# Optimization experiments

Hardware: AMD Instinct MI355X
Metric: run time of the kernel (lower is better)

Reference implementation:

```python
import jax, jax.numpy as jnp
import numpy as np

SEGMENT_LENGTHS = (512, 1024, 2048)
DILATION_RATES = (1, 2, 4)


def _dilated_attention(q, k, v):
    """LongNet-style dilated segment attention.

    Faithful to RingDilatedAttentionHybridFixed._fallback_forward (ring_size=1,
    non-causal, eval mode): for each (segment_length, dilation_rate) pair the
    sequence is tiled into segments; queries attend to K/V gathered at strided
    (dilated) positions start + i*dilation within the sequence; indices past
    seq_len are masked out (the torch code drops them). Each group writes the
    full output buffer, so later groups overwrite earlier ones, exactly as in
    the source loop.
    """
    B, N, H, D = q.shape
    scale = D ** -0.5
    out = jnp.zeros_like(q)
    for seg_len, dil in zip(SEGMENT_LENGTHS, DILATION_RATES):
        seg = min(seg_len, N)
        nseg = N // seg  # N chosen divisible by every segment length
        qg = q.reshape(B, nseg, seg, H, D)
        # dilated kv indices per segment: start + i*dilation  -> [nseg, seg]
        idx = (jnp.arange(nseg) * seg)[:, None] + jnp.arange(seg)[None, :] * dil
        valid = idx < N
        idxc = jnp.minimum(idx, N - 1)
        kg = k[:, idxc]  # [B, nseg, seg, H, D]
        vg = v[:, idxc]
        scores = jnp.einsum('bnqhd,bnkhd->bnhqk', qg, kg) * scale
        scores = jnp.where(valid[None, :, None, None, :], scores, -jnp.inf)
        attn = jax.nn.softmax(scores, axis=-1)
        seg_out = jnp.einsum('bnhqk,bnkhd->bnqhd', attn, vg)
        # each group covers all positions -> whole-output overwrite (as in torch)
        out = seg_out.reshape(B, N, H, D)
    return out


def setup_inputs() -> dict:
    key = jax.random.key(0)
    kq, kk, kv = jax.random.split(key, 3)
    B, N, H, D = 1, 4096, 16, 64
    q = jax.random.normal(kq, (B, N, H, D), dtype=jnp.float32)
    k = jax.random.normal(kk, (B, N, H, D), dtype=jnp.float32)
    v = jax.random.normal(kv, (B, N, H, D), dtype=jnp.float32)
    return {"q": q, "k": k, "v": v}


def reference(q, k, v):
    return _dilated_attention(q, k, v)
```

## Files before the change

### kernel.cpp

```cpp
#include <hip/hip_runtime.h>
#include <hip/hip_bf16.h>
#include <stdint.h>


#define NH   16
#define HD   64
#define KMAX 1024

typedef __attribute__((ext_vector_type(8)))  short s16x8;
typedef __attribute__((ext_vector_type(4)))  float f32x4;
typedef __attribute__((ext_vector_type(16))) float f32x16;

__device__ __forceinline__ uint cvtpk(float lo, float hi) {
    uint r;
    asm("v_cvt_pk_bf16_f32 %0, %1, %2" : "=v"(r) : "v"(lo), "v"(hi));
    return r;
}

__device__ __forceinline__ void swap32(uint& a, uint& b) {
    asm volatile("v_permlane32_swap_b32 %0, %1" : "+v"(a), "+v"(b));
}

__device__ __forceinline__ float fexp2(float x) {
#if __has_builtin(__builtin_amdgcn_exp2f)
    return __builtin_amdgcn_exp2f(x);
#else
    return exp2f(x);
#endif
}

__device__ __forceinline__ void async_load16(const ushort* g, ushort* l) {
    __builtin_amdgcn_global_load_lds(
        (const __attribute__((address_space(1))) void*)g,
        (__attribute__((address_space(3))) void*)l, 16, 0, 0);
}

__device__ __forceinline__ int swz8(int row) { return (row ^ (row >> 3)) & 7; }

__global__ __launch_bounds__(256) void prep_kernel(
    const float* __restrict__ kin, const float* __restrict__ vin,
    ushort* __restrict__ Kb, ushort* __restrict__ Vt)
{
    int bid = blockIdx.x;
    int h   = bid >> 4;
    int ib  = bid & 15;
    int i0  = ib * 64;

    int t  = threadIdx.x;
    int il = t >> 2;
    int d0 = (t & 3) * 16;
    int i  = i0 + il;
    int pos = i * 4;

    const float* ks = kin + (size_t)pos * (NH*HD) + h * HD + d0;
    const float* vs = vin + (size_t)pos * (NH*HD) + h * HD + d0;

    union { uint u[8]; ushort s[16]; uint4 q4[2]; } kb, vb;
    #pragma unroll
    for (int j = 0; j < 4; ++j) {
        float4 a = ((const float4*)ks)[j];
        float4 b = ((const float4*)vs)[j];
        kb.u[2*j]   = cvtpk(a.x, a.y);
        kb.u[2*j+1] = cvtpk(a.z, a.w);
        vb.u[2*j]   = cvtpk(b.x, b.y);
        vb.u[2*j+1] = cvtpk(b.z, b.w);
    }
    size_t kdst = ((size_t)h * KMAX + i) * HD + d0;
    ((uint4*)(Kb + kdst))[0] = kb.q4[0];
    ((uint4*)(Kb + kdst))[1] = kb.q4[1];

    __shared__ ushort vl[64 * 72];
    #pragma unroll
    for (int j = 0; j < 16; ++j) vl[il * 72 + d0 + j] = vb.s[j];
    __syncthreads();

    int d  = t >> 2;
    int ic = (t & 3) * 16;
    __attribute__((aligned(16))) ushort ob[16];
    #pragma unroll
    for (int j = 0; j < 16; ++j) ob[j] = vl[(ic + j) * 72 + d];
    size_t vdst = ((size_t)h * HD + d) * KMAX + i0 + ic;
    ((uint4*)(Vt + vdst))[0] = *(const uint4*)&ob[0];
    ((uint4*)(Vt + vdst))[1] = *(const uint4*)&ob[8];
}

__global__ __launch_bounds__(256, 4) void attn_kernel(
    const float* __restrict__ qin, const ushort* __restrict__ Kb,
    const ushort* __restrict__ Vt, float* __restrict__ outp)
{
    int bid = blockIdx.x;
    int h   = bid & 15;
    int qb  = (bid >> 4) & 31;
    int seg = bid >> 9;
    int NS  = seg ? 4 : 8;

    int tid  = threadIdx.x;
    int wid  = tid >> 6;
    int qg   = wid & 1;
    int kh   = wid >> 1;
    int lane = tid & 63;
    int c    = lane & 31;
    int hi   = lane >> 5;

    __shared__ __attribute__((aligned(16))) ushort smem[2][2][64*64];

    const float QSC = 0.125f * 1.4426950408889634f;
    s16x8 qf[4];
    int qrow = seg*2048 + qb*64 + qg*32 + c;
    {
        const float* qs = qin + (size_t)qrow * (NH*HD) + h*HD;
        #pragma unroll
        for (int s = 0; s < 4; ++s) {
            int dd = 16*s + 8*hi;
            float4 a = *(const float4*)(qs + dd);
            float4 b = *(const float4*)(qs + dd + 4);
            union { uint u[4]; s16x8 v; } r;
            r.u[0] = cvtpk(a.x*QSC, a.y*QSC);
            r.u[1] = cvtpk(a.z*QSC, a.w*QSC);
            r.u[2] = cvtpk(b.x*QSC, b.y*QSC);
            r.u[3] = cvtpk(b.z*QSC, b.w*QSC);
            qf[s] = r.v;
        }
    }

    int kbase = seg*512 + kh*(NS*64);
    const ushort* gsrc[8];
    size_t gstep;
    ushort* ldst;
    {
        int srow = lane >> 3;
        int pc   = lane & 7;
        if (qg == 0) {
            const ushort* gK = Kb + ((size_t)h*KMAX + kbase)*HD;
            #pragma unroll
            for (int cc = 0; cc < 8; ++cc) {
                int row = cc*8 + srow;
                gsrc[cc] = gK + (size_t)row*HD + ((pc ^ swz8(row)) << 3);
            }
            gstep = (size_t)(64*HD);
            ldst  = &smem[kh][0][0];
        } else {
            const ushort* gV = Vt + (size_t)h*HD*KMAX + kbase;
            #pragma unroll
            for (int cc = 0; cc < 8; ++cc) {
                int row = cc*8 + srow;
                gsrc[cc] = gV + (size_t)row*KMAX + ((pc ^ swz8(row)) << 3);
            }
            gstep = (size_t)64;
            ldst  = &smem[kh][1][0];
        }
    }

    f32x16 O[2];
    #pragma unroll
    for (int dg = 0; dg < 2; ++dg)
        #pragma unroll
        for (int i = 0; i < 16; ++i) O[dg][i] = 0.f;
    float l = 0.f;

    const ushort* kbuf = &smem[kh][0][0];
    const ushort* vbuf = &smem[kh][1][0];

    for (int s = 0; s < NS; ++s) {
        {
            size_t off = (size_t)s * gstep;
            #pragma unroll
            for (int cc = 0; cc < 8; ++cc)
                async_load16(gsrc[cc] + off, ldst + cc*512);
        }
        asm volatile("s_waitcnt vmcnt(0)" ::: "memory");
        __builtin_amdgcn_s_barrier();

        #pragma unroll
        for (int kg = 0; kg < 2; ++kg) {
            f32x16 S;
            #pragma unroll
            for (int i = 0; i < 16; ++i) S[i] = 0.f;
            int krow = kg*32 + c;
            int ksw  = swz8(krow);
            #pragma unroll
            for (int s4 = 0; s4 < 4; ++s4) {
                s16x8 af = *(const s16x8*)(kbuf + krow*HD + (((2*s4+hi) ^ ksw) << 3));
                S = __builtin_amdgcn_mfma_f32_32x32x16_bf16(af, qf[s4], S, 0,0,0);
            }
            float p[16];
            #pragma unroll
            for (int i = 0; i < 16; ++i) p[i] = fexp2(S[i]);
            l += (((p[0]+p[1])+(p[2]+p[3])) + ((p[4]+p[5])+(p[6]+p[7])))
               + (((p[8]+p[9])+(p[10]+p[11])) + ((p[12]+p[13])+(p[14]+p[15])));
            uint w0 = cvtpk(p[0],  p[1]),  w1 = cvtpk(p[2],  p[3]);
            uint w2 = cvtpk(p[4],  p[5]),  w3 = cvtpk(p[6],  p[7]);
            uint w4 = cvtpk(p[8],  p[9]),  w5 = cvtpk(p[10], p[11]);
            uint w6 = cvtpk(p[12], p[13]), w7 = cvtpk(p[14], p[15]);
            swap32(w0, w2); swap32(w1, w3);
            swap32(w4, w6); swap32(w5, w7);
            union { uint u[4]; s16x8 v; } b0, b1;
            b0.u[0]=w0; b0.u[1]=w1; b0.u[2]=w2; b0.u[3]=w3;
            b1.u[0]=w4; b1.u[1]=w5; b1.u[2]=w6; b1.u[3]=w7;
            #pragma unroll
            for (int dg = 0; dg < 2; ++dg) {
                int vrow = dg*32 + c;
                int vsw  = swz8(vrow);
                s16x8 v0 = *(const s16x8*)(vbuf + vrow*64 + (((4*kg+hi)   ^ vsw) << 3));
                s16x8 v1 = *(const s16x8*)(vbuf + vrow*64 + (((4*kg+2+hi) ^ vsw) << 3));
                O[dg] = __builtin_amdgcn_mfma_f32_32x32x16_bf16(v0, b0.v, O[dg], 0,0,0);
                O[dg] = __builtin_amdgcn_mfma_f32_32x32x16_bf16(v1, b1.v, O[dg], 0,0,0);
            }
        }

        asm volatile("s_waitcnt lgkmcnt(0)" ::: "memory");
        __builtin_amdgcn_s_barrier();
    }

    l += __shfl_xor(l, 32);

    float* Op = (float*)&smem[0][0][0];
    float* ll = Op + 64*68;
    int qloc = qg*32 + c;
    if (kh == 1) {
        #pragma unroll
        for (int dg = 0; dg < 2; ++dg)
            #pragma unroll
            for (int m = 0; m < 4; ++m) {
                float4 o4 = { O[dg][4*m+0], O[dg][4*m+1], O[dg][4*m+2], O[dg][4*m+3] };
                *(float4*)(Op + qloc*68 + dg*32 + m*8 + 4*hi) = o4;
            }
        if (hi == 0) ll[qloc] = l;
    }
    __syncthreads();
    if (kh == 0) {
        float invl = 1.0f / (l + ll[qloc]);
        float* ob = outp + (size_t)qrow * (NH*HD) + h*HD;
        #pragma unroll
        for (int dg = 0; dg < 2; ++dg)
            #pragma unroll
            for (int m = 0; m < 4; ++m) {
                f32x4 p4 = *(const f32x4*)(Op + qloc*68 + dg*32 + m*8 + 4*hi);
                float4 o4 = { (O[dg][4*m+0]+p4[0])*invl, (O[dg][4*m+1]+p4[1])*invl,
                              (O[dg][4*m+2]+p4[2])*invl, (O[dg][4*m+3]+p4[3])*invl };
                *(float4*)(ob + dg*32 + m*8 + 4*hi) = o4;
            }
    }
}

extern "C" void kernel_launch(void* const* d_in, const int* in_sizes, int n_in,
                              void* d_out, int out_size, void* d_ws, size_t ws_size,
                              hipStream_t stream) {
    const float* q = (const float*)d_in[0];
    const float* k = (const float*)d_in[1];
    const float* v = (const float*)d_in[2];
    float* out = (float*)d_out;

    ushort* Kb = (ushort*)d_ws;
    ushort* Vt = Kb + (size_t)NH * KMAX * HD;

    prep_kernel<<<256, 256, 0, stream>>>(k, v, Kb, Vt);
    attn_kernel<<<1024, 256, 0, stream>>>(q, Kb, Vt, out);
}
```

Baseline: 32.13 us.

## Process 128 query rows per block so each K/V tile feeds two MFMA chains

Each block now handles 128 queries instead of 64, with every wave holding two 32-row query fragments. Each K/V tile loaded into LDS is therefore reused by twice as many MFMAs, and the grid is halved to 512 blocks. The cost is more accumulator registers (launch bounds relaxed to 2 blocks per SIMD) and a two-pass LDS reduction of the partial outputs at the end. s_setprio calls are also added around the MFMA sections to favour matrix issue.

```diff
diff --git a/kernel.cpp b/kernel.cpp
--- a/kernel.cpp
+++ b/kernel.cpp
@@ -84,14 +84,14 @@
     ((uint4*)(Vt + vdst))[1] = *(const uint4*)&ob[8];
 }
 
-__global__ __launch_bounds__(256, 4) void attn_kernel(
+__global__ __launch_bounds__(256, 2) void attn_kernel(
     const float* __restrict__ qin, const ushort* __restrict__ Kb,
     const ushort* __restrict__ Vt, float* __restrict__ outp)
 {
     int bid = blockIdx.x;
     int h   = bid & 15;
-    int qb  = (bid >> 4) & 31;
-    int seg = bid >> 9;
+    int qb  = (bid >> 4) & 15;
+    int seg = bid >> 8;
     int NS  = seg ? 4 : 8;
 
     int tid  = threadIdx.x;
@@ -105,10 +105,11 @@
     __shared__ __attribute__((aligned(16))) ushort smem[2][2][64*64];
 
     const float QSC = 0.125f * 1.4426950408889634f;
-    s16x8 qf[4];
-    int qrow = seg*2048 + qb*64 + qg*32 + c;
-    {
-        const float* qs = qin + (size_t)qrow * (NH*HD) + h*HD;
+    s16x8 qf[2][4];
+    int qrow0 = seg*2048 + qb*128 + qg*64 + c;
+    #pragma unroll
+    for (int q2 = 0; q2 < 2; ++q2) {
+        const float* qs = qin + (size_t)(qrow0 + q2*32) * (NH*HD) + h*HD;
         #pragma unroll
         for (int s = 0; s < 4; ++s) {
             int dd = 16*s + 8*hi;
@@ -119,7 +120,7 @@
             r.u[1] = cvtpk(a.z*QSC, a.w*QSC);
             r.u[2] = cvtpk(b.x*QSC, b.y*QSC);
             r.u[3] = cvtpk(b.z*QSC, b.w*QSC);
-            qf[s] = r.v;
+            qf[q2][s] = r.v;
         }
     }
 
@@ -151,12 +152,14 @@
         }
     }
 
-    f32x16 O[2];
-    #pragma unroll
-    for (int dg = 0; dg < 2; ++dg)
+    f32x16 O[2][2];
+    #pragma unroll
+    for (int q2 = 0; q2 < 2; ++q2)
         #pragma unroll
-        for (int i = 0; i < 16; ++i) O[dg][i] = 0.f;
-    float l = 0.f;
+        for (int dg = 0; dg < 2; ++dg)
+            #pragma unroll
+            for (int i = 0; i < 16; ++i) O[q2][dg][i] = 0.f;
+    float l[2] = {0.f, 0.f};
 
     const ushort* kbuf = &smem[kh][0][0];
     const ushort* vbuf = &smem[kh][1][0];
@@ -173,73 +176,99 @@
 
         #pragma unroll
         for (int kg = 0; kg < 2; ++kg) {
-            f32x16 S;
-            #pragma unroll
-            for (int i = 0; i < 16; ++i) S[i] = 0.f;
+            f32x16 S0, S1;
+            #pragma unroll
+            for (int i = 0; i < 16; ++i) { S0[i] = 0.f; S1[i] = 0.f; }
             int krow = kg*32 + c;
             int ksw  = swz8(krow);
+            __builtin_amdgcn_s_setprio(1);
             #pragma unroll
             for (int s4 = 0; s4 < 4; ++s4) {
                 s16x8 af = *(const s16x8*)(kbuf + krow*HD + (((2*s4+hi) ^ ksw) << 3));
-                S = __builtin_amdgcn_mfma_f32_32x32x16_bf16(af, qf[s4], S, 0,0,0);
-            }
-            float p[16];
-            #pragma unroll
-            for (int i = 0; i < 16; ++i) p[i] = fexp2(S[i]);
-            l += (((p[0]+p[1])+(p[2]+p[3])) + ((p[4]+p[5])+(p[6]+p[7])))
-               + (((p[8]+p[9])+(p[10]+p[11])) + ((p[12]+p[13])+(p[14]+p[15])));
-            uint w0 = cvtpk(p[0],  p[1]),  w1 = cvtpk(p[2],  p[3]);
-            uint w2 = cvtpk(p[4],  p[5]),  w3 = cvtpk(p[6],  p[7]);
-            uint w4 = cvtpk(p[8],  p[9]),  w5 = cvtpk(p[10], p[11]);
-            uint w6 = cvtpk(p[12], p[13]), w7 = cvtpk(p[14], p[15]);
-            swap32(w0, w2); swap32(w1, w3);
-            swap32(w4, w6); swap32(w5, w7);
-            union { uint u[4]; s16x8 v; } b0, b1;
-            b0.u[0]=w0; b0.u[1]=w1; b0.u[2]=w2; b0.u[3]=w3;
-            b1.u[0]=w4; b1.u[1]=w5; b1.u[2]=w6; b1.u[3]=w7;
+                S0 = __builtin_amdgcn_mfma_f32_32x32x16_bf16(af, qf[0][s4], S0, 0,0,0);
+                S1 = __builtin_amdgcn_mfma_f32_32x32x16_bf16(af, qf[1][s4], S1, 0,0,0);
+            }
+            __builtin_amdgcn_s_setprio(0);
+            union { uint u[4]; s16x8 v; } b[2][2];
+            #pragma unroll
+            for (int q2 = 0; q2 < 2; ++q2) {
+                const f32x16& S = q2 ? S1 : S0;
+                float p[16];
+                #pragma unroll
+                for (int i = 0; i < 16; ++i) p[i] = fexp2(S[i]);
+                l[q2] += (((p[0]+p[1])+(p[2]+p[3])) + ((p[4]+p[5])+(p[6]+p[7])))
+                       + (((p[8]+p[9])+(p[10]+p[11])) + ((p[12]+p[13])+(p[14]+p[15])));
+                uint w0 = cvtpk(p[0],  p[1]),  w1 = cvtpk(p[2],  p[3]);
+                uint w2 = cvtpk(p[4],  p[5]),  w3 = cvtpk(p[6],  p[7]);
+                uint w4 = cvtpk(p[8],  p[9]),  w5 = cvtpk(p[10], p[11]);
+                uint w6 = cvtpk(p[12], p[13]), w7 = cvtpk(p[14], p[15]);
+                swap32(w0, w2); swap32(w1, w3);
+                swap32(w4, w6); swap32(w5, w7);
+                b[q2][0].u[0]=w0; b[q2][0].u[1]=w1; b[q2][0].u[2]=w2; b[q2][0].u[3]=w3;
+                b[q2][1].u[0]=w4; b[q2][1].u[1]=w5; b[q2][1].u[2]=w6; b[q2][1].u[3]=w7;
+            }
+            __builtin_amdgcn_s_setprio(1);
             #pragma unroll
             for (int dg = 0; dg < 2; ++dg) {
                 int vrow = dg*32 + c;
                 int vsw  = swz8(vrow);
                 s16x8 v0 = *(const s16x8*)(vbuf + vrow*64 + (((4*kg+hi)   ^ vsw) << 3));
                 s16x8 v1 = *(const s16x8*)(vbuf + vrow*64 + (((4*kg+2+hi) ^ vsw) << 3));
-                O[dg] = __builtin_amdgcn_mfma_f32_32x32x16_bf16(v0, b0.v, O[dg], 0,0,0);
-                O[dg] = __builtin_amdgcn_mfma_f32_32x32x16_bf16(v1, b1.v, O[dg], 0,0,0);
-            }
+                O[0][dg] = __builtin_amdgcn_mfma_f32_32x32x16_bf16(v0, b[0][0].v, O[0][dg], 0,0,0);
+                O[1][dg] = __builtin_amdgcn_mfma_f32_32x32x16_bf16(v0, b[1][0].v, O[1][dg], 0,0,0);
+                O[0][dg] = __builtin_amdgcn_mfma_f32_32x32x16_bf16(v1, b[0][1].v, O[0][dg], 0,0,0);
+                O[1][dg] = __builtin_amdgcn_mfma_f32_32x32x16_bf16(v1, b[1][1].v, O[1][dg], 0,0,0);
+            }
+            __builtin_amdgcn_s_setprio(0);
         }
 
         asm volatile("s_waitcnt lgkmcnt(0)" ::: "memory");
         __builtin_amdgcn_s_barrier();
     }
 
-    l += __shfl_xor(l, 32);
+    #pragma unroll
+    for (int q2 = 0; q2 < 2; ++q2) l[q2] += __shfl_xor(l[q2], 32);
 
     float* Op = (float*)&smem[0][0][0];
     float* ll = Op + 64*68;
-    int qloc = qg*32 + c;
-    if (kh == 1) {
-        #pragma unroll
-        for (int dg = 0; dg < 2; ++dg)
-            #pragma unroll
-            for (int m = 0; m < 4; ++m) {
-                float4 o4 = { O[dg][4*m+0], O[dg][4*m+1], O[dg][4*m+2], O[dg][4*m+3] };
-                *(float4*)(Op + qloc*68 + dg*32 + m*8 + 4*hi) = o4;
-            }
-        if (hi == 0) ll[qloc] = l;
-    }
-    __syncthreads();
-    if (kh == 0) {
-        float invl = 1.0f / (l + ll[qloc]);
-        float* ob = outp + (size_t)qrow * (NH*HD) + h*HD;
-        #pragma unroll
-        for (int dg = 0; dg < 2; ++dg)
-            #pragma unroll
-            for (int m = 0; m < 4; ++m) {
-                f32x4 p4 = *(const f32x4*)(Op + qloc*68 + dg*32 + m*8 + 4*hi);
-                float4 o4 = { (O[dg][4*m+0]+p4[0])*invl, (O[dg][4*m+1]+p4[1])*invl,
-                              (O[dg][4*m+2]+p4[2])*invl, (O[dg][4*m+3]+p4[3])*invl };
-                *(float4*)(ob + dg*32 + m*8 + 4*hi) = o4;
-            }
+    #pragma unroll
+    for (int pass = 0; pass < 2; ++pass) {
+        __syncthreads();
+        if (qg == pass && kh == 1) {
+            #pragma unroll
+            for (int q2 = 0; q2 < 2; ++q2) {
+                int qloc = q2*32 + c;
+                #pragma unroll
+                for (int dg = 0; dg < 2; ++dg)
+                    #pragma unroll
+                    for (int m = 0; m < 4; ++m) {
+                        float4 o4 = { O[q2][dg][4*m+0], O[q2][dg][4*m+1],
+                                      O[q2][dg][4*m+2], O[q2][dg][4*m+3] };
+                        *(float4*)(Op + qloc*68 + dg*32 + m*8 + 4*hi) = o4;
+                    }
+                if (hi == 0) ll[qloc] = l[q2];
+            }
+        }
+        __syncthreads();
+        if (qg == pass && kh == 0) {
+            #pragma unroll
+            for (int q2 = 0; q2 < 2; ++q2) {
+                int qloc = q2*32 + c;
+                float invl = 1.0f / (l[q2] + ll[qloc]);
+                float* ob = outp + (size_t)(qrow0 + q2*32) * (NH*HD) + h*HD;
+                #pragma unroll
+                for (int dg = 0; dg < 2; ++dg)
+                    #pragma unroll
+                    for (int m = 0; m < 4; ++m) {
+                        f32x4 p4 = *(const f32x4*)(Op + qloc*68 + dg*32 + m*8 + 4*hi);
+                        float4 o4 = { (O[q2][dg][4*m+0]+p4[0])*invl,
+                                      (O[q2][dg][4*m+1]+p4[1])*invl,
+                                      (O[q2][dg][4*m+2]+p4[2])*invl,
+                                      (O[q2][dg][4*m+3]+p4[3])*invl };
+                        *(float4*)(ob + dg*32 + m*8 + 4*hi) = o4;
+                    }
+            }
+        }
     }
 }
 
@@ -255,5 +284,5 @@
     ushort* Vt = Kb + (size_t)NH * KMAX * HD;
 
     prep_kernel<<<256, 256, 0, stream>>>(k, v, Kb, Vt);
-    attn_kernel<<<1024, 256, 0, stream>>>(q, Kb, Vt, out);
-}
+    attn_kernel<<<512, 256, 0, stream>>>(q, Kb, Vt, out);
+}
```

After: 32.38 us. About the same (+0.8%).

## Double query rows per block to share staged K/V tiles across more waves

Applied to the files above, without the earlier changes.

Each block now handles 128 query rows with 8 waves (4 query groups by 2 key halves) instead of 64 rows with 4 waves. Each K/V tile staged into shared memory is reused by twice as many query waves, so total K/V traffic from global memory is halved. The copy work per wave drops from 8 to 4 async loads, and the output-merge shared buffer is enlarged to fit 128 rows. The cost is half as many blocks (512) and heavier per-block barriers, which may reduce occupancy and latency hiding.

```diff
diff --git a/kernel.cpp b/kernel.cpp
--- a/kernel.cpp
+++ b/kernel.cpp
@@ -84,29 +84,32 @@
     ((uint4*)(Vt + vdst))[1] = *(const uint4*)&ob[8];
 }
 
-__global__ __launch_bounds__(256, 4) void attn_kernel(
+__global__ __launch_bounds__(512, 4) void attn_kernel(
     const float* __restrict__ qin, const ushort* __restrict__ Kb,
     const ushort* __restrict__ Vt, float* __restrict__ outp)
 {
     int bid = blockIdx.x;
     int h   = bid & 15;
-    int qb  = (bid >> 4) & 31;
-    int seg = bid >> 9;
+    int qc  = (bid >> 4) & 15;
+    int seg = bid >> 8;
     int NS  = seg ? 4 : 8;
 
     int tid  = threadIdx.x;
     int wid  = tid >> 6;
-    int qg   = wid & 1;
-    int kh   = wid >> 1;
+    int qg   = wid & 3;
+    int kh   = wid >> 2;
     int lane = tid & 63;
     int c    = lane & 31;
     int hi   = lane >> 5;
 
-    __shared__ __attribute__((aligned(16))) ushort smem[2][2][64*64];
+    __shared__ __attribute__((aligned(16))) char smraw[35840];
+    ushort* stg = (ushort*)smraw;
+    float*  Op  = (float*)smraw;
+    float*  ll  = (float*)(smraw + 128*68*4);
 
     const float QSC = 0.125f * 1.4426950408889634f;
     s16x8 qf[4];
-    int qrow = seg*2048 + qb*64 + qg*32 + c;
+    int qrow = seg*2048 + qc*128 + qg*32 + c;
     {
         const float* qs = qin + (size_t)qrow * (NH*HD) + h*HD;
         #pragma unroll
@@ -124,32 +127,28 @@
     }
 
     int kbase = seg*512 + kh*(NS*64);
-    const ushort* gsrc[8];
+    const ushort* gsrc[4];
     size_t gstep;
     ushort* ldst;
     {
+        bool isK = (qg < 2);
+        int  qh  = qg & 1;
         int srow = lane >> 3;
         int pc   = lane & 7;
-        if (qg == 0) {
-            const ushort* gK = Kb + ((size_t)h*KMAX + kbase)*HD;
-            #pragma unroll
-            for (int cc = 0; cc < 8; ++cc) {
-                int row = cc*8 + srow;
-                gsrc[cc] = gK + (size_t)row*HD + ((pc ^ swz8(row)) << 3);
-            }
-            gstep = (size_t)(64*HD);
-            ldst  = &smem[kh][0][0];
-        } else {
-            const ushort* gV = Vt + (size_t)h*HD*KMAX + kbase;
-            #pragma unroll
-            for (int cc = 0; cc < 8; ++cc) {
-                int row = cc*8 + srow;
-                gsrc[cc] = gV + (size_t)row*KMAX + ((pc ^ swz8(row)) << 3);
-            }
-            gstep = (size_t)64;
-            ldst  = &smem[kh][1][0];
-        }
-    }
+        const ushort* gbase = isK ? (Kb + ((size_t)h*KMAX + kbase)*HD)
+                                  : (Vt + (size_t)h*HD*KMAX + kbase);
+        size_t rstride = isK ? (size_t)HD : (size_t)KMAX;
+        #pragma unroll
+        for (int cc = 0; cc < 4; ++cc) {
+            int cl  = qh*4 + cc;
+            int row = cl*8 + srow;
+            gsrc[cc] = gbase + (size_t)row*rstride + ((pc ^ swz8(row)) << 3);
+        }
+        gstep = isK ? (size_t)(64*HD) : (size_t)64;
+        ldst  = stg + ((kh*2 + (isK ? 0 : 1))*4096) + qh*4*512;
+    }
+    const ushort* kbuf = stg + (kh*2    )*4096;
+    const ushort* vbuf = stg + (kh*2 + 1)*4096;
 
     f32x16 O[2];
     #pragma unroll
@@ -157,15 +156,12 @@
         #pragma unroll
         for (int i = 0; i < 16; ++i) O[dg][i] = 0.f;
     float l = 0.f;
-
-    const ushort* kbuf = &smem[kh][0][0];
-    const ushort* vbuf = &smem[kh][1][0];
 
     for (int s = 0; s < NS; ++s) {
         {
             size_t off = (size_t)s * gstep;
             #pragma unroll
-            for (int cc = 0; cc < 8; ++cc)
+            for (int cc = 0; cc < 4; ++cc)
                 async_load16(gsrc[cc] + off, ldst + cc*512);
         }
         asm volatile("s_waitcnt vmcnt(0)" ::: "memory");
@@ -214,15 +210,14 @@
 
     l += __shfl_xor(l, 32);
 
-    float* Op = (float*)&smem[0][0][0];
-    float* ll = Op + 64*68;
     int qloc = qg*32 + c;
     if (kh == 1) {
         #pragma unroll
         for (int dg = 0; dg < 2; ++dg)
             #pragma unroll
             for (int m = 0; m < 4; ++m) {
-                float4 o4 = { O[dg][4*m+0], O[dg][4*m+1], O[dg][4*m+2], O[dg][4*m+3] };
+                float4 o4 = { O[dg][4*m+0], O[dg][4*m+1],
+                              O[dg][4*m+2], O[dg][4*m+3] };
                 *(float4*)(Op + qloc*68 + dg*32 + m*8 + 4*hi) = o4;
             }
         if (hi == 0) ll[qloc] = l;
@@ -255,5 +250,5 @@
     ushort* Vt = Kb + (size_t)NH * KMAX * HD;
 
     prep_kernel<<<256, 256, 0, stream>>>(k, v, Kb, Vt);
-    attn_kernel<<<1024, 256, 0, stream>>>(q, Kb, Vt, out);
-}
+    attn_kernel<<<512, 512, 0, stream>>>(q, Kb, Vt, out);
+}
```

Result: faster. 31.49 us (-2.0%).
